# Kernel optimization log

Hardware: AMD Instinct MI355X
Metric: run time of the kernel (lower is better)

## Reference

```python
import jax, jax.numpy as jnp
import numpy as np

# dims
N, T, F, DEMO, H, NHEAD, K, GCN, FFN = 4096, 48, 76, 4, 252, 4, 10, 256, 128
D = H + DEMO          # 256, input dim to graph constructor / clustering / gcn
DK = D // NHEAD       # 64
TAU, MASK_P, LAMBDA_KL, LAMBDA_CL, PHI_INIT, ALPHA = 0.5, 0.1, 1.0, 1.0, 3.0 / N, 1.0


def setup_inputs() -> dict:
    key = jax.random.key(0)
    ks = jax.random.split(key, 16)
    s = 0.02
    return dict(
        x=jax.random.normal(ks[0], (N, T, F), jnp.float32),
        x_demo=jax.random.normal(ks[1], (N, DEMO), jnp.float32),
        sorted_length=jax.random.randint(ks[2], (N,), 1, T + 1),
        mask_edge=jax.random.uniform(ks[3], (N, N), jnp.float32),
        w_ih=jax.random.normal(ks[4], (3 * H, F), jnp.float32) * s,
        w_hh=jax.random.normal(ks[5], (3 * H, H), jnp.float32) * s,
        b_ih=jnp.zeros((3 * H,), jnp.float32),
        b_hh=jnp.zeros((3 * H,), jnp.float32),
        h0=jnp.zeros((H,), jnp.float32),
        wq=jax.random.normal(ks[6], (D, D), jnp.float32) * s,
        bq=jnp.zeros((D,), jnp.float32),
        wk=jax.random.normal(ks[7], (D, D), jnp.float32) * s,
        bk=jnp.zeros((D,), jnp.float32),
        wo=jax.random.normal(ks[8], (NHEAD,), jnp.float32) * s,
        bo=jnp.zeros((), jnp.float32),
        phi=jnp.float32(PHI_INIT),
        centers=jax.random.normal(ks[9], (K, D), jnp.float32),
        gcn_w=jax.random.normal(ks[10], (D, GCN), jnp.float32) * s,
        gcn_b=jnp.zeros((GCN,), jnp.float32),
        ffn_w=jax.random.normal(ks[11], (GCN, FFN), jnp.float32) * s,
        ffn_b=jnp.zeros((FFN,), jnp.float32),
        pre_w=jax.random.normal(ks[12], (GCN, 2), jnp.float32) * s,
        pre_b=jnp.zeros((2,), jnp.float32),
    )


def _forward(x, x_demo, sorted_length, mask_edge, w_ih, w_hh, b_ih, b_hh, h0,
             wq, bq, wk, bk, wo, bo, phi, centers, gcn_w, gcn_b,
             ffn_w, ffn_b, pre_w, pre_b):
    n = x.shape[0]

    # --- GRU over time (torch nn.GRU equations), scan over T ---
    def gru_step(h, xt):
        gi = xt @ w_ih.T + b_ih                     # [N, 3H]
        gh = h @ w_hh.T + b_hh
        ir, iz, inn = jnp.split(gi, 3, axis=-1)
        hr, hz, hn = jnp.split(gh, 3, axis=-1)
        r = jax.nn.sigmoid(ir + hr)
        zg = jax.nn.sigmoid(iz + hz)
        ng = jnp.tanh(inn + r * hn)
        h = (1.0 - zg) * ng + zg * h
        return h, h

    _, outs = jax.lax.scan(gru_step, jnp.broadcast_to(h0, (n, H)), jnp.swapaxes(x, 0, 1))
    idx = jnp.clip(sorted_length - 1, 0, T - 1)
    x_gru = outs[idx, jnp.arange(n)]                # last valid hidden state [N, H]
    x_star = jnp.concatenate([x_gru, x_demo], axis=1)  # [N, D]

    # --- GraphConstructor: multi-head attention adjacency ---
    q = (x_star @ wq.T + bq).reshape(n, NHEAD, DK)
    kk = (x_star @ wk.T + bk).reshape(n, NHEAD, DK)
    scores = jnp.einsum('nhd,mhd->nmh', q, kk) / np.sqrt(DK)  # [N, N, h]
    scores = scores @ wo + bo                                  # Wo: Linear(h, 1)
    attn = jax.nn.softmax(scores, axis=1)
    eye = jnp.eye(n, dtype=x.dtype)
    adj = jnp.where(attn >= phi, 1.0, 0.0) * (1.0 - eye)       # threshold, zero diag

    # --- Clustering: soft assignment around given centers (KMeans fit replaced
    #     by fixed cluster_layer parameter; same soft-assign / KLD math) ---
    d2 = jnp.sum((x_star[:, None, :] - centers[None]) ** 2, axis=-1)  # [N, K]
    qsoft = 1.0 / (1.0 + d2 / ALPHA)
    qsoft = qsoft / jnp.sum(qsoft, axis=1, keepdims=True)
    pdist = qsoft ** 2 / jnp.sum(qsoft, axis=0, keepdims=True)
    pdist = jax.lax.stop_gradient(pdist / jnp.sum(pdist, axis=1, keepdims=True))
    label = jnp.argmax(qsoft, axis=1)
    kl_loss = jnp.mean(jnp.sum(pdist * jnp.log(pdist / (qsoft + 1e-6)), axis=-1))

    # --- GCNConv on dense adjacency (sym-normalized with self loops) ---
    xw = x_star @ gcn_w

    def gcn(a):
        a_hat = a + eye
        dinv = 1.0 / jnp.sqrt(jnp.sum(a_hat, axis=1))
        return (dinv[:, None] * a_hat * dinv[None, :]) @ xw + gcn_b

    z = gcn(adj)
    adj_aug = adj * (mask_edge >= MASK_P).astype(x.dtype)  # DataAug edge mask (bernoulli keep 1-p)
    z_aug = gcn(adj_aug)
    zf = z @ ffn_w + ffn_b
    zfa = z_aug @ ffn_w + ffn_b

    # --- clloss: NxN contrastive loss ---
    def l2n(a):
        return a / jnp.clip(jnp.linalg.norm(a, axis=1, keepdims=True), 1e-12, None)

    zn, zan = l2n(zf), l2n(zfa)
    intra = jnp.exp(zn @ zn.T / TAU)
    inter = jnp.exp(zn @ zan.T / TAU)
    cadj = (label[:, None] == label[None, :]).astype(x.dtype) * (1.0 - eye)
    cadj_new = jnp.where(adj == 1.0, 0.0, cadj)
    positive = jnp.diag(inter) + jnp.sum(intra * adj, axis=1) + jnp.sum(intra * cadj_new, axis=1)
    denom = jnp.sum(intra, axis=1) + jnp.sum(inter, axis=1) - jnp.diag(intra)
    cnt = jnp.sum(adj, axis=1) + jnp.sum(cadj_new, axis=1) + 1.0
    cl_loss = -jnp.sum(jnp.log(positive / denom) / cnt)

    loss = LAMBDA_KL * kl_loss + LAMBDA_CL * cl_loss
    output = z @ pre_w + pre_b
    return output, loss


def reference(x, x_demo, sorted_length, mask_edge, w_ih, w_hh, b_ih, b_hh, h0,
              wq, bq, wk, bk, wo, bo, phi, centers, gcn_w, gcn_b,
              ffn_w, ffn_b, pre_w, pre_b):
    return _forward(x, x_demo, sorted_length, mask_edge, w_ih, w_hh, b_ih, b_hh, h0,
                    wq, bq, wk, bk, wo, bo, phi, centers, gcn_w, gcn_b,
                    ffn_w, ffn_b, pre_w, pre_b)
```

## Files before the change

kernel.cpp:

```cpp
#include <hip/hip_runtime.h>
#include <cstdint>
#include <cstddef>

typedef _Float16 f16;
typedef f16 f16x8 __attribute__((ext_vector_type(8)));
typedef float f32x4 __attribute__((ext_vector_type(4)));

#define MFMA(a,b,c) __builtin_amdgcn_mfma_f32_16x16x32_f16(a,b,c,0,0,0)

__device__ __forceinline__ float sigm(float x){ return 1.f/(1.f+__expf(-x)); }
__device__ __forceinline__ float tanh_f(float x){
  float a = __expf(-2.f*fabsf(x));
  float t = (1.f-a)/(1.f+a);
  return x >= 0.f ? t : -t;
}
__device__ __forceinline__ uint16_t f2bf(float f){
  uint32_t u = __float_as_uint(f);
  return (uint16_t)((u + 0x7fffu + ((u>>16)&1u)) >> 16);
}
__device__ __forceinline__ float bf2f(uint16_t h){
  return __uint_as_float(((uint32_t)h) << 16);
}

__global__ __launch_bounds__(256) void k_prep(
    const float* __restrict__ w_ih, const float* __restrict__ w_hh,
    const float* __restrict__ b_ih, const float* __restrict__ b_hh,
    const int* __restrict__ slen,
    const float* __restrict__ wq, const float* __restrict__ wk,
    const float* __restrict__ gcn_w,
    f16* __restrict__ BgT, f16* __restrict__ wq16, f16* __restrict__ wk16,
    f16* __restrict__ gw16, float* __restrict__ biasc, int* __restrict__ idx)
{
  int id = blockIdx.x*256 + threadIdx.x;
  if (id < 360448){
    int g = id / (256*352); int rem = id % (256*352);
    int j = rem / 352; int k = rem % 352;
    float v = 0.f;
    if (j < 252){
      if (k < 96){
        if (k < 76 && g != 3){
          int row = (g==2) ? (504+j) : (g*252+j);
          v = w_ih[row*76 + k];
        }
      } else {
        int kh = k - 96;
        if (kh < 252 && g != 2){
          int row = (g==3) ? (504+j) : (g*252+j);
          v = w_hh[row*252 + kh];
        }
      }
    }
    BgT[id] = (f16)v;
    return;
  }
  id -= 360448;
  if (id < 65536){ wq16[id] = (f16)wq[id]; return; }
  id -= 65536;
  if (id < 65536){ wk16[id] = (f16)wk[id]; return; }
  id -= 65536;
  if (id < 65536){ int j = id >> 8, d = id & 255; gw16[id] = (f16)gcn_w[d*256 + j]; return; }
  id -= 65536;
  if (id < 1008){
    int g = id / 252, j = id % 252; float v;
    if (g==0) v = b_ih[j] + b_hh[j];
    else if (g==1) v = b_ih[252+j] + b_hh[252+j];
    else if (g==2) v = b_ih[504+j];
    else v = b_hh[504+j];
    biasc[id] = v; return;
  }
  id -= 1008;
  if (id < 4096){
    int s = slen[id] - 1; s = s < 0 ? 0 : (s > 47 ? 47 : s);
    idx[id] = s; return;
  }
}

__global__ __launch_bounds__(256) void k_xt(const float* __restrict__ x,
    f16* __restrict__ x16t)
{
  int id = blockIdx.x*256 + threadIdx.x;
  int c = id % 12; int rem = id / 12;
  int n = rem & 4095; int t = rem >> 12;
  const float* xp = x + ((size_t)n*48 + t)*76;
  f16x8 o;
  #pragma unroll
  for (int e = 0; e < 8; ++e){
    int k = c*8 + e;
    o[e] = (k < 76) ? (f16)xp[k] : (f16)0.f;
  }
  *(f16x8*)(x16t + ((size_t)t*4096 + n)*96 + c*8) = o;
}

__global__ __launch_bounds__(1024, 4) void k_gru_all(
    const f16* __restrict__ x16t, const f16* __restrict__ BgT,
    const float* __restrict__ biasc, const float* __restrict__ h0,
    const int* __restrict__ idxp, float* __restrict__ xstar)
{
  __shared__ f16 hbuf[2][32][256];
  __shared__ int idxl[32];
  int lane = threadIdx.x & 63, w = threadIdx.x >> 6;
  int l16 = lane & 15, lq = lane >> 4;
  int nb = blockIdx.x * 32;

  for (int i = threadIdx.x; i < 32*256; i += 1024){
    int row = i >> 8, c = i & 255;
    int sc = (((c >> 3) ^ (row & 7)) << 3) | (c & 7);
    hbuf[0][row][sc] = (c < 252) ? (f16)h0[c] : (f16)0.f;
  }
  if (threadIdx.x < 32) idxl[threadIdx.x] = idxp[nb + threadIdx.x];

  int j = w*16 + l16;
  bool jv = (j < 252);
  int js = jv ? j : 251;
  float bR = biasc[js], bZ = biasc[252+js], bI = biasc[504+js], bH = biasc[756+js];
  const f16* pR = BgT + (size_t)(0*256 + j)*352 + lq*8;
  const f16* pZ = BgT + (size_t)(1*256 + j)*352 + lq*8;
  const f16* pI = BgT + (size_t)(2*256 + j)*352 + lq*8;
  const f16* pH = BgT + (size_t)(3*256 + j)*352 + lq*8;
  const f16* xp0 = x16t + ((size_t)nb + l16)*96 + lq*8;
  const f16* xp1 = x16t + ((size_t)nb + 16 + l16)*96 + lq*8;

  float hown[2][4];
  #pragma unroll
  for (int mf = 0; mf < 2; ++mf)
  #pragma unroll
  for (int r = 0; r < 4; ++r)
    hown[mf][r] = jv ? h0[js] : 0.f;

  __syncthreads();

  for (int t = 0; t < 48; ++t){
    const f16 (*hin)[256] = hbuf[t & 1];
    f16 (*hout)[256]      = hbuf[(t & 1) ^ 1];
    f32x4 z4 = {0.f,0.f,0.f,0.f};
    f32x4 aR[2] = {z4,z4}, aZ[2] = {z4,z4}, aI[2] = {z4,z4}, aH[2] = {z4,z4};
    size_t xt = (size_t)t*4096*96;

    f16x8 wR[11], wZ[11], wM[11];
    #define LW(u_) do{ \
      wR[u_] = *(const f16x8*)(pR + (u_)*32); \
      wZ[u_] = *(const f16x8*)(pZ + (u_)*32); \
      wM[u_] = ((u_) < 3) ? *(const f16x8*)(pI + (u_)*32) \
                          : *(const f16x8*)(pH + (u_)*32); }while(0)
    LW(0); LW(1);
    #pragma unroll
    for (int u = 0; u < 11; ++u){
      if (u + 2 < 11) LW(u + 2);
      f16x8 a0, a1;
      if (u < 3){
        a0 = *(const f16x8*)(xp0 + xt + u*32);
        a1 = *(const f16x8*)(xp1 + xt + u*32);
      } else {
        int chunk = (u - 3)*4 + lq;
        a0 = *(const f16x8*)(&hin[l16][(chunk ^ (l16 & 7)) << 3]);
        a1 = *(const f16x8*)(&hin[16 + l16][(chunk ^ (l16 & 7)) << 3]);
      }
      aR[0] = MFMA(a0, wR[u], aR[0]);  aR[1] = MFMA(a1, wR[u], aR[1]);
      aZ[0] = MFMA(a0, wZ[u], aZ[0]);  aZ[1] = MFMA(a1, wZ[u], aZ[1]);
      if (u < 3){ aI[0] = MFMA(a0, wM[u], aI[0]);  aI[1] = MFMA(a1, wM[u], aI[1]); }
      else      { aH[0] = MFMA(a0, wM[u], aH[0]);  aH[1] = MFMA(a1, wM[u], aH[1]); }
    }
    #undef LW

    #pragma unroll
    for (int mf = 0; mf < 2; ++mf)
    #pragma unroll
    for (int r = 0; r < 4; ++r){
      int row = mf*16 + lq*4 + r;
      float rr = sigm(aR[mf][r] + bR);
      float zz = sigm(aZ[mf][r] + bZ);
      float ng = tanh_f(aI[mf][r] + bI + rr*(aH[mf][r] + bH));
      float hnew = (1.f - zz)*ng + zz*hown[mf][r];
      hnew = jv ? hnew : 0.f;
      hown[mf][r] = hnew;
      int sc = (((j >> 3) ^ (row & 7)) << 3) | (j & 7);
      hout[row][sc] = (f16)hnew;
      if (jv && idxl[row] == t) xstar[((size_t)(nb + row) << 8) + j] = hnew;
    }
    __syncthreads();
  }
}

__global__ __launch_bounds__(256) void k_xstar(const float* __restrict__ x_demo,
    float* __restrict__ xs32, f16* __restrict__ xs16)
{
  int id = blockIdx.x*256 + threadIdx.x;
  int n = id >> 8, c = id & 255;
  float v;
  if (c < 252) v = xs32[id];
  else v = x_demo[n*4 + (c - 252)];
  xs32[id] = v;
  xs16[id] = (f16)v;
}

template<int MODE>
__global__ __launch_bounds__(256) void k_proj(const f16* __restrict__ xs16,
    const f16* __restrict__ w16, const float* __restrict__ bias,
    const float* __restrict__ wo, f16* __restrict__ out16)
{
  int lane = threadIdx.x & 63, wv = threadIdx.x >> 6;
  int l16 = lane & 15, lq = lane >> 4;
  int nb = blockIdx.x * 64;
  int ocol = blockIdx.y*64 + wv*16 + l16;
  f32x4 z4 = {0.f,0.f,0.f,0.f};
  f32x4 acc[4] = {z4,z4,z4,z4};
  #pragma unroll
  for (int ks = 0; ks < 8; ++ks){
    f16x8 b = *(const f16x8*)(w16 + (size_t)ocol*256 + ks*32 + lq*8);
    #pragma unroll
    for (int mi = 0; mi < 4; ++mi){
      f16x8 a = *(const f16x8*)(xs16 + (size_t)(nb + mi*16 + l16)*256 + ks*32 + lq*8);
      acc[mi] = MFMA(a, b, acc[mi]);
    }
  }
  float badd = bias[ocol];
  float scale = (MODE == 0) ? wo[ocol >> 6]*0.125f : 1.f;
  #pragma unroll
  for (int mi = 0; mi < 4; ++mi)
  #pragma unroll
  for (int r = 0; r < 4; ++r){
    int n = nb + mi*16 + lq*4 + r;
    float v = acc[mi][r] + badd;
    if (MODE == 0) v *= scale;
    out16[(size_t)n*256 + ocol] = (f16)v;
  }
}

__global__ __launch_bounds__(256) void k_scores(const f16* __restrict__ qf,
    const f16* __restrict__ kf, uint16_t* __restrict__ sco)
{
  int lane = threadIdx.x & 63, w = threadIdx.x >> 6;
  int l16 = lane & 15, lq = lane >> 4;
  int mh = w >> 1, jh = w & 1;
  int nb = blockIdx.x*128 + mh*64;
  int mb = blockIdx.y*128 + jh*64;
  f32x4 z4 = {0.f,0.f,0.f,0.f};
  f32x4 acc[4][4];
  #pragma unroll
  for (int i = 0; i < 4; ++i)
  #pragma unroll
  for (int j = 0; j < 4; ++j) acc[i][j] = z4;
  #pragma unroll
  for (int ks = 0; ks < 8; ++ks){
    f16x8 a[4], b[4];
    #pragma unroll
    for (int i = 0; i < 4; ++i){
      a[i] = *(const f16x8*)(qf + (size_t)(nb + i*16 + l16)*256 + ks*32 + lq*8);
      b[i] = *(const f16x8*)(kf + (size_t)(mb + i*16 + l16)*256 + ks*32 + lq*8);
    }
    #pragma unroll
    for (int mi = 0; mi < 4; ++mi)
    #pragma unroll
    for (int jf = 0; jf < 4; ++jf)
      acc[mi][jf] = MFMA(a[mi], b[jf], acc[mi][jf]);
  }
  #pragma unroll
  for (int mi = 0; mi < 4; ++mi)
  #pragma unroll
  for (int jf = 0; jf < 4; ++jf)
  #pragma unroll
  for (int r = 0; r < 4; ++r){
    int n = nb + mi*16 + lq*4 + r;
    int m = mb + jf*16 + l16;
    sco[((size_t)n << 12) + m] = f2bf(acc[mi][jf][r]);
  }
}

__global__ __launch_bounds__(256) void k_adj(const uint16_t* __restrict__ sco,
    const float* __restrict__ mask_edge, const float* __restrict__ phip,
    uint8_t* __restrict__ flags, float* __restrict__ sadj,
    float* __restrict__ dinv, float* __restrict__ dinva)
{
  int n = blockIdx.x;
  int lane = threadIdx.x & 63, wv = threadIdx.x >> 6;
  const uint16_t* row = sco + ((size_t)n << 12);
  int base = threadIdx.x * 16;
  const uint4* p = (const uint4*)(row + base);
  uint4 w0 = p[0], w1 = p[1];
  uint32_t ws_[8] = {w0.x,w0.y,w0.z,w0.w,w1.x,w1.y,w1.z,w1.w};
  float v[16];
  #pragma unroll
  for (int i = 0; i < 8; ++i){
    v[2*i]   = bf2f((uint16_t)(ws_[i] & 0xffffu));
    v[2*i+1] = bf2f((uint16_t)(ws_[i] >> 16));
  }
  float mx = v[0];
  #pragma unroll
  for (int i = 1; i < 16; ++i) mx = fmaxf(mx, v[i]);
  #pragma unroll
  for (int o = 32; o >= 1; o >>= 1) mx = fmaxf(mx, __shfl_xor(mx, o));
  __shared__ float redA[4], redB[4], redC[4], redD[4];
  if (lane == 0) redA[wv] = mx;
  __syncthreads();
  mx = fmaxf(fmaxf(redA[0], redA[1]), fmaxf(redA[2], redA[3]));
  float s = 0.f;
  #pragma unroll
  for (int i = 0; i < 16; ++i) s += __expf(v[i] - mx);
  #pragma unroll
  for (int o = 32; o >= 1; o >>= 1) s += __shfl_xor(s, o);
  if (lane == 0) redB[wv] = s;
  __syncthreads();
  float rs = 1.f / (redB[0] + redB[1] + redB[2] + redB[3]);
  float phi = phip[0];
  uint32_t by[16]; int c0 = 0, c1 = 0;
  #pragma unroll
  for (int e = 0; e < 16; ++e){
    float a = __expf(v[e] - mx) * rs;
    int col = base + e;
    uint32_t b = (a >= phi && col != n) ? 1u : 0u;
    if (b){ if (mask_edge[((size_t)n << 12) + col] >= 0.1f) b |= 2u; }
    by[e] = b;
    c0 += (int)(b & 1u);
    c1 += (int)(b >> 1);
  }
  uint4 pk;
  pk.x = by[0]  | (by[1]  << 8) | (by[2]  << 16) | (by[3]  << 24);
  pk.y = by[4]  | (by[5]  << 8) | (by[6]  << 16) | (by[7]  << 24);
  pk.z = by[8]  | (by[9]  << 8) | (by[10] << 16) | (by[11] << 24);
  pk.w = by[12] | (by[13] << 8) | (by[14] << 16) | (by[15] << 24);
  *(uint4*)(flags + ((size_t)n << 12) + base) = pk;
  float f0 = (float)c0, f1 = (float)c1;
  #pragma unroll
  for (int o = 32; o >= 1; o >>= 1){ f0 += __shfl_xor(f0, o); f1 += __shfl_xor(f1, o); }
  if (lane == 0){ redC[wv] = f0; redD[wv] = f1; }
  __syncthreads();
  if (threadIdx.x == 0){
    float d0 = redC[0]+redC[1]+redC[2]+redC[3];
    float d1 = redD[0]+redD[1]+redD[2]+redD[3];
    sadj[n] = d0;
    dinv[n]  = rsqrtf(1.f + d0);
    dinva[n] = rsqrtf(1.f + d1);
  }
}

__global__ __launch_bounds__(256) void k_xw_y(const f16* __restrict__ xs16,
    const f16* __restrict__ gw16, const float* __restrict__ dinv,
    const float* __restrict__ dinva, f16* __restrict__ y16, f16* __restrict__ ya16)
{
  int lane = threadIdx.x & 63, wv = threadIdx.x >> 6;
  int l16 = lane & 15, lq = lane >> 4;
  int nb = blockIdx.x * 64;
  int jcol = blockIdx.y*64 + wv*16 + l16;
  f32x4 z4 = {0.f,0.f,0.f,0.f};
  f32x4 acc[4] = {z4,z4,z4,z4};
  #pragma unroll
  for (int ks = 0; ks < 8; ++ks){
    f16x8 b = *(const f16x8*)(gw16 + (size_t)jcol*256 + ks*32 + lq*8);
    #pragma unroll
    for (int mi = 0; mi < 4; ++mi){
      f16x8 a = *(const f16x8*)(xs16 + (size_t)(nb + mi*16 + l16)*256 + ks*32 + lq*8);
      acc[mi] = MFMA(a, b, acc[mi]);
    }
  }
  #pragma unroll
  for (int mi = 0; mi < 4; ++mi)
  #pragma unroll
  for (int r = 0; r < 4; ++r){
    int n = nb + mi*16 + lq*4 + r;
    float v = acc[mi][r];
    y16[(size_t)n*256 + jcol]  = (f16)(dinv[n]*v);
    ya16[(size_t)n*256 + jcol] = (f16)(dinva[n]*v);
  }
}

__global__ __launch_bounds__(256) void k_zgather(const uint8_t* __restrict__ flags,
    const f16* __restrict__ y16, const f16* __restrict__ ya16,
    const float* __restrict__ dinv, const float* __restrict__ dinva,
    const float* __restrict__ gcn_b, float* __restrict__ z32, float* __restrict__ za32)
{
  int n = blockIdx.x;
  int lane = threadIdx.x & 63, wv = threadIdx.x >> 6;
  uint4 w = ((const uint4*)(flags + ((size_t)n << 12)))[threadIdx.x];
  uint32_t m0[4] = {w.x & 0x01010101u, w.y & 0x01010101u, w.z & 0x01010101u, w.w & 0x01010101u};
  uint32_t m1[4] = {w.x & 0x02020202u, w.y & 0x02020202u, w.z & 0x02020202u, w.w & 0x02020202u};
  int c0 = __popc(m0[0]) + __popc(m0[1]) + __popc(m0[2]) + __popc(m0[3]);
  int c1 = __popc(m1[0]) + __popc(m1[1]) + __popc(m1[2]) + __popc(m1[3]);
  int v0 = c0, v1 = c1;
  #pragma unroll
  for (int o = 1; o < 64; o <<= 1){
    int u0 = __shfl_up(v0, o), u1 = __shfl_up(v1, o);
    if (lane >= o){ v0 += u0; v1 += u1; }
  }
  __shared__ int wsum0[4], wsum1[4];
  if (lane == 63){ wsum0[wv] = v0; wsum1[wv] = v1; }
  __syncthreads();
  int pos0 = v0 - c0, pos1 = v1 - c1;
  #pragma unroll
  for (int i = 0; i < 4; ++i) if (i < wv){ pos0 += wsum0[i]; pos1 += wsum1[i]; }
  int tot0 = wsum0[0]+wsum0[1]+wsum0[2]+wsum0[3];
  int tot1 = wsum1[0]+wsum1[1]+wsum1[2]+wsum1[3];
  __shared__ uint16_t list0[4096];
  __shared__ uint16_t list1[4096];
  int cbase = threadIdx.x * 16;
  #pragma unroll
  for (int q = 0; q < 4; ++q){
    uint32_t m = m0[q];
    while (m){
      int b = __ffs(m) - 1;
      list0[pos0++] = (uint16_t)(cbase + q*4 + (b >> 3));
      m &= m - 1;
    }
    m = m1[q];
    while (m){
      int b = __ffs(m) - 1;
      list1[pos1++] = (uint16_t)(cbase + q*4 + (b >> 3));
      m &= m - 1;
    }
  }
  __syncthreads();
  int j = threadIdx.x;
  float acc0 = (float)y16[((size_t)n << 8) + j];
  float acc1 = (float)ya16[((size_t)n << 8) + j];
  for (int i = 0; i < tot0; ++i) acc0 += (float)y16[((size_t)list0[i] << 8) + j];
  for (int i = 0; i < tot1; ++i) acc1 += (float)ya16[((size_t)list1[i] << 8) + j];
  z32[((size_t)n << 8) + j]  = dinv[n]*acc0 + gcn_b[j];
  za32[((size_t)n << 8) + j] = dinva[n]*acc1 + gcn_b[j];
}

__global__ __launch_bounds__(256) void k_cluster(const float* __restrict__ xs32,
    const float* __restrict__ centers, float* __restrict__ qsoft,
    int* __restrict__ labels, float* __restrict__ colsum)
{
  int nb = blockIdx.x * 16;
  __shared__ float xs[16][256];
  __shared__ float ct[2560];
  __shared__ float d2s[16][10];
  __shared__ float qs[16][10];
  for (int i = threadIdx.x; i < 16*256; i += 256) xs[i >> 8][i & 255] = xs32[(size_t)nb*256 + i];
  for (int i = threadIdx.x; i < 2560; i += 256){ int k = i >> 8, d = i & 255; ct[d*10 + k] = centers[i]; }
  __syncthreads();
  if (threadIdx.x < 160){
    int r = threadIdx.x / 10, k = threadIdx.x % 10;
    float s = 0.f;
    for (int d = 0; d < 256; ++d){ float df = xs[r][d] - ct[d*10 + k]; s += df*df; }
    d2s[r][k] = s;
  }
  __syncthreads();
  if (threadIdx.x < 16){
    int r = threadIdx.x;
    float un[10]; float tot = 0.f;
    #pragma unroll
    for (int k = 0; k < 10; ++k){ un[k] = 1.f/(1.f + d2s[r][k]); tot += un[k]; }
    float inv = 1.f / tot;
    int best = 0; float bm = un[0];
    #pragma unroll
    for (int k = 1; k < 10; ++k){ if (un[k] > bm){ bm = un[k]; best = k; } }
    labels[nb + r] = best;
    #pragma unroll
    for (int k = 0; k < 10; ++k){ float q = un[k]*inv; qs[r][k] = q; qsoft[(size_t)(nb + r)*10 + k] = q; }
  }
  __syncthreads();
  if (threadIdx.x < 10){
    int k = threadIdx.x; float s = 0.f;
    #pragma unroll
    for (int r = 0; r < 16; ++r) s += qs[r][k];
    atomicAdd(&colsum[k], s);
  }
}

__global__ __launch_bounds__(256) void k_kl(const float* __restrict__ qsoft,
    const float* __restrict__ colsum, float* __restrict__ klsum)
{
  int n = blockIdx.x*256 + threadIdx.x;
  float p[10]; float s = 0.f;
  #pragma unroll
  for (int k = 0; k < 10; ++k){
    float q = qsoft[(size_t)n*10 + k];
    float pu = q*q/colsum[k];
    p[k] = pu; s += pu;
  }
  float inv = 1.f/s; float kl = 0.f;
  #pragma unroll
  for (int k = 0; k < 10; ++k){
    float pk = p[k]*inv;
    float q = qsoft[(size_t)n*10 + k];
    kl += pk*__logf(pk/(q + 1e-6f));
  }
  int lane = threadIdx.x & 63, wv = threadIdx.x >> 6;
  #pragma unroll
  for (int o = 32; o >= 1; o >>= 1) kl += __shfl_xor(kl, o);
  __shared__ float red[4];
  if (lane == 0) red[wv] = kl;
  __syncthreads();
  if (threadIdx.x == 0) atomicAdd(klsum, red[0]+red[1]+red[2]+red[3]);
}

__global__ __launch_bounds__(128) void k_ffn(const float* __restrict__ z32,
    const float* __restrict__ za32, const float* __restrict__ ffn_w,
    const float* __restrict__ ffn_b, f16* __restrict__ zn16, f16* __restrict__ zan16)
{
  int n = blockIdx.x; int aug = blockIdx.y;
  const float* z = (aug ? za32 : z32) + ((size_t)n << 8);
  __shared__ float zr[256];
  zr[threadIdx.x] = z[threadIdx.x];
  zr[threadIdx.x + 128] = z[threadIdx.x + 128];
  __syncthreads();
  int j = threadIdx.x;
  float acc = ffn_b[j];
  #pragma unroll 8
  for (int d = 0; d < 256; ++d) acc += zr[d]*ffn_w[d*128 + j];
  float ss = acc*acc;
  int lane = threadIdx.x & 63, wv = threadIdx.x >> 6;
  #pragma unroll
  for (int o = 32; o >= 1; o >>= 1) ss += __shfl_xor(ss, o);
  __shared__ float sred[2];
  if (lane == 0) sred[wv] = ss;
  __syncthreads();
  float tot = sred[0] + sred[1];
  float rn = 1.f / fmaxf(sqrtf(tot), 1e-12f);
  (aug ? zan16 : zn16)[((size_t)n << 7) + j] = (f16)(acc*rn);
}

__global__ __launch_bounds__(256) void k_closs(const f16* __restrict__ zn,
    const f16* __restrict__ zan, const uint8_t* __restrict__ flags,
    const int* __restrict__ labels,
    float* __restrict__ rs1, float* __restrict__ rs2, float* __restrict__ rsA,
    float* __restrict__ rsC, float* __restrict__ rcC, float* __restrict__ rdI,
    float* __restrict__ rdi)
{
  int lane = threadIdx.x & 63;
  int ji = threadIdx.x >> 6;
  int l16 = lane & 15, lq = lane >> 4;
  int nb = blockIdx.x * 32;
  int mstart = blockIdx.y * 512;
  f16x8 A[2][4];
  #pragma unroll
  for (int mi = 0; mi < 2; ++mi)
  #pragma unroll
  for (int ks = 0; ks < 4; ++ks)
    A[mi][ks] = *(const f16x8*)(zn + (size_t)(nb + mi*16 + l16)*128 + ks*32 + lq*8);
  int labn[8];
  #pragma unroll
  for (int i = 0; i < 8; ++i) labn[i] = labels[nb + (i >> 2)*16 + lq*4 + (i & 3)];
  float a1[8]={}, a2[8]={}, aA[8]={}, aC[8]={}, aCc[8]={}, adI[8]={}, adi[8]={};
  for (int tile = 0; tile < 8; ++tile){
    int mcol = mstart + tile*64 + ji*16 + l16;
    uint8_t flv[8];
    #pragma unroll
    for (int i = 0; i < 8; ++i){
      int n = nb + (i >> 2)*16 + lq*4 + (i & 3);
      flv[i] = flags[((size_t)n << 12) + mcol];
    }
    int labm = labels[mcol];
    f32x4 z4 = {0.f,0.f,0.f,0.f};
    f32x4 acc1[2] = {z4, z4};
    f32x4 acc2[2] = {z4, z4};
    #pragma unroll
    for (int ks = 0; ks < 4; ++ks){
      f16x8 b1 = *(const f16x8*)(zn  + (size_t)mcol*128 + ks*32 + lq*8);
      f16x8 b2 = *(const f16x8*)(zan + (size_t)mcol*128 + ks*32 + lq*8);
      #pragma unroll
      for (int mi = 0; mi < 2; ++mi){
        acc1[mi] = MFMA(A[mi][ks], b1, acc1[mi]);
        acc2[mi] = MFMA(A[mi][ks], b2, acc2[mi]);
      }
    }
    #pragma unroll
    for (int mi = 0; mi < 2; ++mi)
    #pragma unroll
    for (int r = 0; r < 4; ++r){
      int i8 = mi*4 + r;
      int n = nb + mi*16 + lq*4 + r;
      float e1 = __expf(2.f*acc1[mi][r]);
      float e2 = __expf(2.f*acc2[mi][r]);
      uint8_t fl = flv[i8];
      a1[i8] += e1; a2[i8] += e2;
      bool adjb = (fl & 1);
      if (adjb) aA[i8] += e1;
      if (!adjb && labn[i8] == labm && n != mcol){ aC[i8] += e1; aCc[i8] += 1.f; }
      if (n == mcol){ adI[i8] += e2; adi[i8] += e1; }
    }
  }
  #pragma unroll
  for (int i = 0; i < 8; ++i){
    #pragma unroll
    for (int o = 1; o < 16; o <<= 1){
      a1[i]  += __shfl_xor(a1[i], o);  a2[i]  += __shfl_xor(a2[i], o);
      aA[i]  += __shfl_xor(aA[i], o);  aC[i]  += __shfl_xor(aC[i], o);
      aCc[i] += __shfl_xor(aCc[i], o); adI[i] += __shfl_xor(adI[i], o);
      adi[i] += __shfl_xor(adi[i], o);
    }
  }
  if (l16 == 0){
    #pragma unroll
    for (int i = 0; i < 8; ++i){
      int n = nb + (i >> 2)*16 + lq*4 + (i & 3);
      atomicAdd(&rs1[n], a1[i]);  atomicAdd(&rs2[n], a2[i]);
      atomicAdd(&rsA[n], aA[i]);  atomicAdd(&rsC[n], aC[i]);
      atomicAdd(&rcC[n], aCc[i]); atomicAdd(&rdI[n], adI[i]);
      atomicAdd(&rdi[n], adi[i]);
    }
  }
}

__global__ __launch_bounds__(256) void k_clfinal(const float* __restrict__ rs1,
    const float* __restrict__ rs2, const float* __restrict__ rsA,
    const float* __restrict__ rsC, const float* __restrict__ rcC,
    const float* __restrict__ rdI, const float* __restrict__ rdi,
    const float* __restrict__ sadj, float* __restrict__ clsum)
{
  int n = blockIdx.x*256 + threadIdx.x;
  float pos = rdI[n] + rsA[n] + rsC[n];
  float den = rs1[n] + rs2[n] - rdi[n];
  float cnt = sadj[n] + rcC[n] + 1.f;
  float v = __logf(pos/den)/cnt;
  int lane = threadIdx.x & 63, wv = threadIdx.x >> 6;
  #pragma unroll
  for (int o = 32; o >= 1; o >>= 1) v += __shfl_xor(v, o);
  __shared__ float red[4];
  if (lane == 0) red[wv] = v;
  __syncthreads();
  if (threadIdx.x == 0) atomicAdd(clsum, red[0]+red[1]+red[2]+red[3]);
}

__global__ void k_loss(const float* __restrict__ scal, float* __restrict__ out){
  out[8192] = scal[0]*(1.f/4096.f) - scal[1];
}

__global__ __launch_bounds__(256) void k_outhead(const float* __restrict__ z32,
    const float* __restrict__ pre_w, const float* __restrict__ pre_b,
    float* __restrict__ out)
{
  int lane = threadIdx.x & 63, wv = threadIdx.x >> 6;
  int n = blockIdx.x*4 + wv;
  float4 zv = *(const float4*)(z32 + ((size_t)n << 8) + lane*4);
  float4 w0 = *(const float4*)(pre_w + lane*8);
  float4 w1 = *(const float4*)(pre_w + lane*8 + 4);
  float c0 = zv.x*w0.x + zv.y*w0.z + zv.z*w1.x + zv.w*w1.z;
  float c1 = zv.x*w0.y + zv.y*w0.w + zv.z*w1.y + zv.w*w1.w;
  #pragma unroll
  for (int o = 32; o >= 1; o >>= 1){ c0 += __shfl_xor(c0, o); c1 += __shfl_xor(c1, o); }
  if (lane == 0){
    out[(size_t)n*2]     = c0 + pre_b[0];
    out[(size_t)n*2 + 1] = c1 + pre_b[1];
  }
}

extern "C" void kernel_launch(void* const* d_in, const int* in_sizes, int n_in,
                              void* d_out, int out_size, void* d_ws, size_t ws_size,
                              hipStream_t stream)
{
  const float* x         = (const float*)d_in[0];
  const float* x_demo    = (const float*)d_in[1];
  const int*   slen      = (const int*)d_in[2];
  const float* mask_edge = (const float*)d_in[3];
  const float* w_ih      = (const float*)d_in[4];
  const float* w_hh      = (const float*)d_in[5];
  const float* b_ih      = (const float*)d_in[6];
  const float* b_hh      = (const float*)d_in[7];
  const float* h0        = (const float*)d_in[8];
  const float* wq        = (const float*)d_in[9];
  const float* bq        = (const float*)d_in[10];
  const float* wk        = (const float*)d_in[11];
  const float* bk        = (const float*)d_in[12];
  const float* wo        = (const float*)d_in[13];
  const float* phi       = (const float*)d_in[15];
  const float* centers   = (const float*)d_in[16];
  const float* gcn_w     = (const float*)d_in[17];
  const float* gcn_b     = (const float*)d_in[18];
  const float* ffn_w     = (const float*)d_in[19];
  const float* ffn_b     = (const float*)d_in[20];
  const float* pre_w     = (const float*)d_in[21];
  const float* pre_b     = (const float*)d_in[22];
  float* out = (float*)d_out;

  size_t off = 0;
  char* base = (char*)d_ws;
  auto take = [&](size_t bytes)->void*{
    void* p = base + off;
    off += (bytes + 255) & ~(size_t)255;
    return p;
  };
  f16*   BgT    = (f16*)take((size_t)4*256*352*2);
  f16*   wq16   = (f16*)take((size_t)65536*2);
  f16*   wk16   = (f16*)take((size_t)65536*2);
  f16*   gw16   = (f16*)take((size_t)65536*2);
  float* biasc  = (float*)take(1008*4);
  int*   idx    = (int*)take(4096*4);
  float* xs32   = (float*)take((size_t)4096*256*4);
  f16*   xs16   = (f16*)take((size_t)4096*256*2);
  f16*   qf16   = (f16*)take((size_t)4096*256*2);
  f16*   kf16   = (f16*)take((size_t)4096*256*2);
  uint16_t* sco = (uint16_t*)take((size_t)4096*4096*2);
  uint8_t* flags= (uint8_t*)take((size_t)4096*4096);
  float* sadj   = (float*)take(4096*4);
  float* dinv   = (float*)take(4096*4);
  float* dinva  = (float*)take(4096*4);
  f16*   y16    = (f16*)take((size_t)4096*256*2);
  f16*   ya16   = (f16*)take((size_t)4096*256*2);
  float* z32    = (float*)take((size_t)4096*256*4);
  float* za32   = (float*)take((size_t)4096*256*4);
  f16*   zn16   = (f16*)take((size_t)4096*128*2);
  f16*   zan16  = (f16*)take((size_t)4096*128*2);
  float* qsoft  = (float*)take((size_t)4096*10*4);
  int*   labels = (int*)take(4096*4);
  float* colsum = (float*)take(64);
  float* scal   = (float*)take(64);
  float* rsbuf  = (float*)take((size_t)7*4096*4);
  float* rs1 = rsbuf,        *rs2 = rsbuf + 4096, *rsA = rsbuf + 2*4096;
  float* rsC = rsbuf + 3*4096, *rcC = rsbuf + 4*4096;
  float* rdI = rsbuf + 5*4096, *rdi = rsbuf + 6*4096;

  f16* x16t = (f16*)sco;

  hipMemsetAsync(colsum, 0, 64, stream);
  hipMemsetAsync(scal, 0, 64, stream);
  hipMemsetAsync(rsbuf, 0, (size_t)7*4096*4, stream);

  k_prep<<<2196, 256, 0, stream>>>(w_ih, w_hh, b_ih, b_hh, slen, wq, wk, gcn_w,
                                   BgT, wq16, wk16, gw16, biasc, idx);
  k_xt<<<9216, 256, 0, stream>>>(x, x16t);
  k_gru_all<<<128, 1024, 0, stream>>>(x16t, BgT, biasc, h0, idx, xs32);
  k_xstar<<<4096, 256, 0, stream>>>(x_demo, xs32, xs16);
  k_proj<0><<<dim3(64, 4), 256, 0, stream>>>(xs16, wq16, bq, wo, qf16);
  k_proj<1><<<dim3(64, 4), 256, 0, stream>>>(xs16, wk16, bk, wo, kf16);
  k_scores<<<dim3(32, 32), 256, 0, stream>>>(qf16, kf16, sco);
  k_adj<<<4096, 256, 0, stream>>>(sco, mask_edge, phi, flags, sadj, dinv, dinva);
  k_xw_y<<<dim3(64, 4), 256, 0, stream>>>(xs16, gw16, dinv, dinva, y16, ya16);
  k_zgather<<<4096, 256, 0, stream>>>(flags, y16, ya16, dinv, dinva, gcn_b, z32, za32);
  k_cluster<<<256, 256, 0, stream>>>(xs32, centers, qsoft, labels, colsum);
  k_kl<<<16, 256, 0, stream>>>(qsoft, colsum, &scal[0]);
  k_ffn<<<dim3(4096, 2), 128, 0, stream>>>(z32, za32, ffn_w, ffn_b, zn16, zan16);
  k_closs<<<dim3(128, 8), 256, 0, stream>>>(zn16, zan16, flags, labels,
                                            rs1, rs2, rsA, rsC, rcC, rdI, rdi);
  k_clfinal<<<16, 256, 0, stream>>>(rs1, rs2, rsA, rsC, rcC, rdI, rdi, sadj, &scal[1]);
  k_loss<<<1, 1, 0, stream>>>(scal, out);
  k_outhead<<<1024, 256, 0, stream>>>(z32, pre_w, pre_b, out);

  (void)in_sizes; (void)n_in; (void)out_size; (void)ws_size;
}
```

Before: 999.3 us.

## Stream GRU weights via global_load_lds double buffer instead of registers

The GRU recurrence kernel now stages per-step weight fragments into a per-wave double-buffered LDS region using direct global-to-LDS loads. It issues them two chunks ahead and uses explicit vmcnt/lgkmcnt waits before reading them back. The aim is to cut VGPR pressure from holding 33 weight vectors and to overlap weight fetch with MFMA work. In exchange it adds about 96KB of shared memory per block and manual waitcnt synchronisation, which may limit occupancy or be fragile if the compiler reorders other memory ops.

```diff
diff --git a/kernel.cpp b/kernel.cpp
--- a/kernel.cpp
+++ b/kernel.cpp
@@ -97,6 +97,7 @@
     const int* __restrict__ idxp, float* __restrict__ xstar)
 {
   __shared__ f16 hbuf[2][32][256];
+  __shared__ f16 wbuf[2][16][3][512];
   __shared__ int idxl[32];
   int lane = threadIdx.x & 63, w = threadIdx.x >> 6;
   int l16 = lane & 15, lq = lane >> 4;
@@ -119,6 +120,7 @@
   const f16* pH = BgT + (size_t)(3*256 + j)*352 + lq*8;
   const f16* xp0 = x16t + ((size_t)nb + l16)*96 + lq*8;
   const f16* xp1 = x16t + ((size_t)nb + 16 + l16)*96 + lq*8;
+  const f16* wrd = &wbuf[0][w][0][lane*8];
 
   float hown[2][4];
   #pragma unroll
@@ -128,6 +130,15 @@
     hown[mf][r] = jv ? h0[js] : 0.f;
 
   __syncthreads();
+
+  #define ISSUE(u_) do{ \
+    __builtin_amdgcn_global_load_lds((const void*)(pR + (u_)*32), \
+        (void*)&wbuf[(u_)&1][w][0][0], 16, 0, 0); \
+    __builtin_amdgcn_global_load_lds((const void*)(pZ + (u_)*32), \
+        (void*)&wbuf[(u_)&1][w][1][0], 16, 0, 0); \
+    __builtin_amdgcn_global_load_lds((const void*)((((u_) < 3) ? pI : pH) + (u_)*32), \
+        (void*)&wbuf[(u_)&1][w][2][0], 16, 0, 0); \
+  }while(0)
 
   for (int t = 0; t < 48; ++t){
     const f16 (*hin)[256] = hbuf[t & 1];
@@ -136,16 +147,15 @@
     f32x4 aR[2] = {z4,z4}, aZ[2] = {z4,z4}, aI[2] = {z4,z4}, aH[2] = {z4,z4};
     size_t xt = (size_t)t*4096*96;
 
-    f16x8 wR[11], wZ[11], wM[11];
-    #define LW(u_) do{ \
-      wR[u_] = *(const f16x8*)(pR + (u_)*32); \
-      wZ[u_] = *(const f16x8*)(pZ + (u_)*32); \
-      wM[u_] = ((u_) < 3) ? *(const f16x8*)(pI + (u_)*32) \
-                          : *(const f16x8*)(pH + (u_)*32); }while(0)
-    LW(0); LW(1);
+    ISSUE(0); ISSUE(1);
     #pragma unroll
     for (int u = 0; u < 11; ++u){
-      if (u + 2 < 11) LW(u + 2);
+      if (u < 10) asm volatile("s_waitcnt vmcnt(3)" ::: "memory");
+      else        asm volatile("s_waitcnt vmcnt(0)" ::: "memory");
+      const f16* wb = wrd + (u & 1)*(16*3*512);
+      f16x8 wR = *(const f16x8*)(wb);
+      f16x8 wZ = *(const f16x8*)(wb + 512);
+      f16x8 wM = *(const f16x8*)(wb + 1024);
       f16x8 a0, a1;
       if (u < 3){
         a0 = *(const f16x8*)(xp0 + xt + u*32);
@@ -155,12 +165,14 @@
         a0 = *(const f16x8*)(&hin[l16][(chunk ^ (l16 & 7)) << 3]);
         a1 = *(const f16x8*)(&hin[16 + l16][(chunk ^ (l16 & 7)) << 3]);
       }
-      aR[0] = MFMA(a0, wR[u], aR[0]);  aR[1] = MFMA(a1, wR[u], aR[1]);
-      aZ[0] = MFMA(a0, wZ[u], aZ[0]);  aZ[1] = MFMA(a1, wZ[u], aZ[1]);
-      if (u < 3){ aI[0] = MFMA(a0, wM[u], aI[0]);  aI[1] = MFMA(a1, wM[u], aI[1]); }
-      else      { aH[0] = MFMA(a0, wM[u], aH[0]);  aH[1] = MFMA(a1, wM[u], aH[1]); }
-    }
-    #undef LW
+      asm volatile("s_waitcnt lgkmcnt(0)" ::: "memory");
+      __builtin_amdgcn_sched_barrier(0);
+      if (u + 2 <= 10) ISSUE(u + 2);
+      aR[0] = MFMA(a0, wR, aR[0]);  aR[1] = MFMA(a1, wR, aR[1]);
+      aZ[0] = MFMA(a0, wZ, aZ[0]);  aZ[1] = MFMA(a1, wZ, aZ[1]);
+      if (u < 3){ aI[0] = MFMA(a0, wM, aI[0]);  aI[1] = MFMA(a1, wM, aI[1]); }
+      else      { aH[0] = MFMA(a0, wM, aH[0]);  aH[1] = MFMA(a1, wM, aH[1]); }
+    }
 
     #pragma unroll
     for (int mf = 0; mf < 2; ++mf)
@@ -179,6 +191,7 @@
     }
     __syncthreads();
   }
+  #undef ISSUE
 }
 
 __global__ __launch_bounds__(256) void k_xstar(const float* __restrict__ x_demo,
```

Result: slower. 1.087 ms (+8.8%).
